# Optimization experiments

Hardware: AMD Instinct MI355X
Metric: run time of the kernel (lower is better)

## Reference

```python
import jax, jax.numpy as jnp
import numpy as np
import math

KEY_SIZE = 128  # init arg; scale = 1/sqrt(key_size)


def setup_inputs() -> dict:
    key = jax.random.key(0)
    kq, kk, kv = jax.random.split(key, 3)
    B, LQ, LK, D, DV = 16, 2048, 2048, 128, 128
    q = jax.random.normal(kq, (B, LQ, D), dtype=jnp.float32)
    k = jax.random.normal(kk, (B, LK, D), dtype=jnp.float32)
    v = jax.random.normal(kv, (B, LK, DV), dtype=jnp.float32)
    return {"q": q, "k": k, "v": v}


def reference(q, k, v):
    scale = 1.0 / math.sqrt(KEY_SIZE)
    # scores: [B, Lq, Lk]
    scores = jnp.einsum('bqd,bkd->bqk', q, k) * scale
    probs = jax.nn.softmax(scores, axis=-1)
    # dropout with p=0.0 is identity (eval-equivalent)
    return jnp.einsum('bqk,bkv->bqv', probs, v)
```

## Files before the change

kernel.cpp:

```cpp
#include <hip/hip_runtime.h>
#include <hip/hip_bf16.h>

typedef float f32x4 __attribute__((ext_vector_type(4)));
typedef float f32x16 __attribute__((ext_vector_type(16)));
typedef short bf16x8 __attribute__((ext_vector_type(8)));
typedef unsigned u32x4 __attribute__((ext_vector_type(4)));

constexpr int NB = 16, LQ = 2048, LK = 2048, D = 128, DV = 128;
constexpr int NTH = 32;
constexpr float SCALE = 0.08838834764831843f;
constexpr float LOG2E = 1.4426950408889634f;
constexpr float QSCALE = SCALE * LOG2E;
constexpr float SHIFT = 12.0f;

__device__ __forceinline__ unsigned short f2bfs(float f) {
  __hip_bfloat16 h = __float2bfloat16(f);
  return __builtin_bit_cast(unsigned short, h);
}

__device__ __forceinline__ unsigned short f2bf(float f) {
  unsigned int u = __float_as_uint(f);
  u += 0x7FFFu + ((u >> 16) & 1u);
  return (unsigned short)(u >> 16);
}

__device__ __forceinline__ int swz2(int row) {
  return (row ^ (row >> 1) ^ (row >> 3)) & 7;
}

__device__ __forceinline__ int swap23(int m) {
  return (m & ~12) | ((m & 4) << 1) | ((m & 8) >> 1);
}

typedef const __attribute__((address_space(1))) void* gas1_t;
typedef __attribute__((address_space(3))) void* las3_t;
__device__ __forceinline__ void gload16(const void* g, void* l) {
  __builtin_amdgcn_global_load_lds((gas1_t)g, (las3_t)l, 16, 0, 0);
}

__device__ __forceinline__ unsigned pk2(float lo, float hi) {
  unsigned short a = f2bfs(lo), b = f2bfs(hi);
  return (unsigned)a | ((unsigned)b << 16);
}

__device__ __forceinline__ void mk_pb(const f32x16& s, bf16x8& pe, bf16x8& po) {
  u32x4 e = {pk2(s[0], s[1]), pk2(s[2], s[3]), pk2(s[4], s[5]), pk2(s[6], s[7])};
  pe = __builtin_bit_cast(bf16x8, e);
  u32x4 od = {pk2(s[8], s[9]), pk2(s[10], s[11]), pk2(s[12], s[13]), pk2(s[14], s[15])};
  po = __builtin_bit_cast(bf16x8, od);
}

__global__ __launch_bounds__(256) void conv_k2(const float* __restrict__ kp,
                                               unsigned short* __restrict__ out) {
  __shared__ __align__(16) unsigned short tk[4096];
  const int T = blockIdx.x, b = blockIdx.y;
  const int tid = threadIdx.x;
  const int k = tid >> 3, cc = tid & 7, d0 = cc * 16;
  const float* src = kp + ((long)(b * LK) + 32 * T + k) * D + d0;
  f32x4 a0 = ((const f32x4*)src)[0];
  f32x4 a1 = ((const f32x4*)src)[1];
  f32x4 a2 = ((const f32x4*)src)[2];
  f32x4 a3 = ((const f32x4*)src)[3];
  bf16x8 r0, r1;
  #pragma unroll
  for (int j = 0; j < 4; ++j) {
    r0[j] = (short)f2bfs(a0[j]); r0[4 + j] = (short)f2bfs(a1[j]);
    r1[j] = (short)f2bfs(a2[j]); r1[4 + j] = (short)f2bfs(a3[j]);
  }
  const int rr = swap23(k);
  *(bf16x8*)&tk[(2 * cc) * 256 + rr * 8] = r0;
  *(bf16x8*)&tk[(2 * cc + 1) * 256 + rr * 8] = r1;
  __syncthreads();
  unsigned short* dst = out + ((long)(b * 64 + T)) * 4096 + tid * 16;
  *(bf16x8*)dst = *(const bf16x8*)&tk[tid * 16];
  *(bf16x8*)(dst + 8) = *(const bf16x8*)&tk[tid * 16 + 8];
}

__global__ __launch_bounds__(256) void conv_v2(const float* __restrict__ vp,
                                               unsigned short* __restrict__ out) {
  __shared__ __align__(16) unsigned short tv[4096];
  const int T = blockIdx.x, b = blockIdx.y;
  const int tid = threadIdx.x;
  const int k = tid >> 3, cc = tid & 7, d0 = cc * 16;
  const float* src = vp + ((long)(b * LK) + 32 * T + k) * DV + d0;
  f32x4 a0 = ((const f32x4*)src)[0];
  f32x4 a1 = ((const f32x4*)src)[1];
  f32x4 a2 = ((const f32x4*)src)[2];
  f32x4 a3 = ((const f32x4*)src)[3];
  unsigned short vals[16];
  #pragma unroll
  for (int j = 0; j < 4; ++j) {
    vals[j]      = f2bfs(a0[j]);
    vals[4 + j]  = f2bfs(a1[j]);
    vals[8 + j]  = f2bfs(a2[j]);
    vals[12 + j] = f2bfs(a3[j]);
  }
  const int vbase = (k >> 3) * 1024 + (k & 7);
  #pragma unroll
  for (int i = 0; i < 16; ++i)
    tv[vbase + (d0 + i) * 8] = vals[i];
  __syncthreads();
  unsigned short* dst = out + ((long)(b * 64 + T)) * 4096 + tid * 16;
  *(bf16x8*)dst = *(const bf16x8*)&tv[tid * 16];
  *(bf16x8*)(dst + 8) = *(const bf16x8*)&tv[tid * 16 + 8];
}

__global__ __launch_bounds__(256, 2) void attn_fwd9(
    const float* __restrict__ qp, const unsigned short* __restrict__ wsK2,
    const unsigned short* __restrict__ wsV2, float* __restrict__ op) {
  __shared__ __align__(16) unsigned short sm[32768];

  const int tid = threadIdx.x;
  const int wid = tid >> 6;
  const int h2  = wid >> 1;
  const int lane = tid & 63;
  const int q32 = lane & 31;
  const int hi  = lane >> 5;
  const int ht  = tid & 127;

  const int bid = blockIdx.x;
  const int sbid = (bid & 7) * 64 + (bid >> 3);
  const int b = sbid >> 5;
  const int qb = (sbid & 31) * 64;
  const int qwave = qb + (wid & 1) * 32;

  bf16x8 aq[8];
  {
    const float* qrow = qp + ((long)(b * LQ + qwave + q32)) * D + hi * 8;
    #pragma unroll
    for (int st = 0; st < 8; ++st) {
      f32x4 x0 = *(const f32x4*)(qrow + st * 16);
      f32x4 x1 = *(const f32x4*)(qrow + st * 16 + 4);
      #pragma unroll
      for (int j = 0; j < 4; ++j) {
        aq[st][j]     = (short)f2bfs(x0[j] * QSCALE);
        aq[st][4 + j] = (short)f2bfs(x1[j] * QSCALE);
      }
    }
  }
  __builtin_amdgcn_sched_barrier(0);

  const int lbase = h2 * 16384;
  const unsigned short* kps = wsK2 + ((long)(b * 64 + h2 * 32)) * 4096;
  const unsigned short* vps = wsV2 + ((long)(b * 64 + h2 * 32)) * 4096;

  auto stage = [&](int buf, int t) {
    const long toff = (long)t * 4096;
    const int lb = lbase + buf * 8192;
    #pragma unroll
    for (int it = 0; it < 4; ++it) {
      const int ci = it * 128 + ht;
      gload16(kps + toff + ci * 8, &sm[lb + ci * 8]);
    }
    #pragma unroll
    for (int it = 0; it < 4; ++it) {
      const int ci = it * 128 + ht;
      gload16(vps + toff + ci * 8, &sm[lb + 4096 + ci * 8]);
    }
  };

  stage(0, 0);
  stage(1, 1);

  f32x16 o[4];
  #pragma unroll
  for (int mt = 0; mt < 4; ++mt) o[mt] = (f32x16){};
  float l_s = 0.f;

  const int kub = lbase + hi * 256 + q32 * 8;
  const int vub = lbase + 4096 + hi * 1024 + q32 * 8;

  asm volatile("s_waitcnt vmcnt(8)" ::: "memory");
  __builtin_amdgcn_sched_barrier(0);
  __builtin_amdgcn_s_barrier();
  __builtin_amdgcn_sched_barrier(0);

  f32x16 s_cur;
  #pragma unroll
  for (int i = 0; i < 16; ++i) s_cur[i] = -SHIFT;
  #pragma unroll
  for (int st = 0; st < 8; ++st) {
    bf16x8 k0 = *(const bf16x8*)&sm[kub + st * 512];
    s_cur = __builtin_amdgcn_mfma_f32_32x32x16_bf16(k0, aq[st], s_cur, 0, 0, 0);
  }
  bf16x8 vf[8];
  #pragma unroll
  for (int ks = 0; ks < 2; ++ks)
    #pragma unroll
    for (int mt = 0; mt < 4; ++mt)
      vf[ks * 4 + mt] = *(const bf16x8*)&sm[vub + ks * 2048 + mt * 256];

  asm volatile("s_waitcnt lgkmcnt(0)" ::: "memory");
  __builtin_amdgcn_sched_barrier(0);
  __builtin_amdgcn_s_barrier();
  __builtin_amdgcn_sched_barrier(0);
  stage(0, 2);

  for (int t = 1; t < NTH; ++t) {
    if (t < NTH - 1) {
      asm volatile("s_waitcnt vmcnt(8)" ::: "memory");
    } else {
      asm volatile("s_waitcnt vmcnt(0)" ::: "memory");
    }
    __builtin_amdgcn_sched_barrier(0);
    __builtin_amdgcn_s_barrier();
    __builtin_amdgcn_sched_barrier(0);

    const int cur = t & 1;
    const int kb = kub + cur * 8192;
    const int vb = vub + cur * 8192;

    f32x16 s_new;
    #pragma unroll
    for (int i = 0; i < 16; ++i) s_new[i] = -SHIFT;
    __builtin_amdgcn_s_setprio(1);
    #pragma unroll
    for (int st = 0; st < 8; ++st) {
      bf16x8 k0 = *(const bf16x8*)&sm[kb + st * 512];
      s_new = __builtin_amdgcn_mfma_f32_32x32x16_bf16(k0, aq[st], s_new, 0, 0, 0);
    }
    __builtin_amdgcn_s_setprio(0);

    #pragma unroll
    for (int i = 0; i < 16; ++i) s_cur[i] = exp2f(s_cur[i]);
    float s8[8];
    #pragma unroll
    for (int i = 0; i < 8; ++i) s8[i] = s_cur[i] + s_cur[i + 8];
    float sum = ((s8[0] + s8[1]) + (s8[2] + s8[3])) +
                ((s8[4] + s8[5]) + (s8[6] + s8[7]));
    l_s += sum + __shfl_xor(sum, 32);
    bf16x8 pb0, pb1;
    mk_pb(s_cur, pb0, pb1);

    __builtin_amdgcn_s_setprio(1);
    #pragma unroll
    for (int mt = 0; mt < 4; ++mt)
      o[mt] = __builtin_amdgcn_mfma_f32_32x32x16_bf16(vf[mt], pb0, o[mt], 0, 0, 0);
    #pragma unroll
    for (int mt = 0; mt < 4; ++mt)
      o[mt] = __builtin_amdgcn_mfma_f32_32x32x16_bf16(vf[4 + mt], pb1, o[mt], 0, 0, 0);
    __builtin_amdgcn_s_setprio(0);

    #pragma unroll
    for (int ks = 0; ks < 2; ++ks)
      #pragma unroll
      for (int mt = 0; mt < 4; ++mt)
        vf[ks * 4 + mt] = *(const bf16x8*)&sm[vb + ks * 2048 + mt * 256];

    asm volatile("s_waitcnt lgkmcnt(0)" ::: "memory");
    __builtin_amdgcn_sched_barrier(0);
    __builtin_amdgcn_s_barrier();
    __builtin_amdgcn_sched_barrier(0);
    if (t + 2 < NTH) stage(cur, t + 2);

    s_cur = s_new;
  }

  {
    #pragma unroll
    for (int i = 0; i < 16; ++i) s_cur[i] = exp2f(s_cur[i]);
    float s8[8];
    #pragma unroll
    for (int i = 0; i < 8; ++i) s8[i] = s_cur[i] + s_cur[i + 8];
    float sum = ((s8[0] + s8[1]) + (s8[2] + s8[3])) +
                ((s8[4] + s8[5]) + (s8[6] + s8[7]));
    l_s += sum + __shfl_xor(sum, 32);
    bf16x8 pb0, pb1;
    mk_pb(s_cur, pb0, pb1);
    #pragma unroll
    for (int mt = 0; mt < 4; ++mt)
      o[mt] = __builtin_amdgcn_mfma_f32_32x32x16_bf16(vf[mt], pb0, o[mt], 0, 0, 0);
    #pragma unroll
    for (int mt = 0; mt < 4; ++mt)
      o[mt] = __builtin_amdgcn_mfma_f32_32x32x16_bf16(vf[4 + mt], pb1, o[mt], 0, 0, 0);
  }

  float* scr = (float*)sm;
  float* wreg = scr + (size_t)(wid & 1) * 4352;
  __syncthreads();
  if (h2 == 1) {
    #pragma unroll
    for (int j4 = 0; j4 < 16; ++j4) {
      const int mt = j4 >> 2, a = j4 & 3;
      f32x4 v = {o[mt][4 * a], o[mt][4 * a + 1], o[mt][4 * a + 2], o[mt][4 * a + 3]};
      *(f32x4*)&wreg[lane * 64 + ((j4 ^ (lane & 15)) << 2)] = v;
    }
    wreg[4096 + lane] = l_s;
  }
  __syncthreads();
  if (h2 == 0) {
    const float l1 = wreg[4096 + lane];
    const float inv = 1.f / (l_s + l1);
    float* dst = op + ((long)(b * LQ + qwave + q32)) * DV;
    #pragma unroll
    for (int j4 = 0; j4 < 16; ++j4) {
      const int mt = j4 >> 2, a = j4 & 3;
      f32x4 pv = *(const f32x4*)&wreg[lane * 64 + ((j4 ^ (lane & 15)) << 2)];
      f32x4 r;
      #pragma unroll
      for (int i = 0; i < 4; ++i) r[i] = (o[mt][4 * a + i] + pv[i]) * inv;
      *(f32x4*)&dst[32 * mt + 8 * a + 4 * hi] = r;
    }
  }
}

__device__ __forceinline__ int swzc(int row, int c16) {
  return c16 ^ ((row ^ (row >> 3)) & 7);
}

__global__ __launch_bounds__(256, 2) void attn_fwd(
    const float* __restrict__ qp, const float* __restrict__ kp,
    const float* __restrict__ vp, float* __restrict__ op) {
  __shared__ __align__(16) unsigned short smm[28672];
  const int tid = threadIdx.x, wid = tid >> 6, lane = tid & 63;
  const int g = lane >> 4, c = lane & 15;
  const int b = blockIdx.y, qb = blockIdx.x * 64;
  const float* qg = qp + ((long)b * LQ + qb) * D;
  const float* kg = kp + (long)b * LK * D;
  const float* vg = vp + (long)b * LK * DV;
  #pragma unroll
  for (int it = 0; it < 4; ++it) {
    int ch = it * 256 + tid, row = ch >> 4, c16 = ch & 15;
    const float* src = qg + row * D + c16 * 8;
    f32x4 f0 = *(const f32x4*)(src);
    f32x4 f1 = *(const f32x4*)(src + 4);
    bf16x8 fr;
    #pragma unroll
    for (int j = 0; j < 4; ++j) {
      fr[j] = (short)f2bf(f0[j] * SCALE);
      fr[4 + j] = (short)f2bf(f1[j] * SCALE);
    }
    *(bf16x8*)&smm[row * 128 + swzc(row, c16) * 8] = fr;
  }
  __syncthreads();
  bf16x8 aq[4];
  #pragma unroll
  for (int ks = 0; ks < 4; ++ks) {
    int row = wid * 16 + c;
    aq[ks] = *(const bf16x8*)&smm[row * 128 + swzc(row, ks * 4 + g) * 8];
  }
  f32x4 o[8]; f32x4 fz = {0.f, 0.f, 0.f, 0.f};
  #pragma unroll
  for (int i = 0; i < 8; ++i) o[i] = fz;
  float m_r[4] = {-1e30f, -1e30f, -1e30f, -1e30f};
  float l_r[4] = {0.f, 0.f, 0.f, 0.f};
  const int pbase = 24576 + wid * 1024;
  for (int kv0 = 0; kv0 < LK; kv0 += 64) {
    __syncthreads();
    const float* ksrc = kg + (long)kv0 * D;
    #pragma unroll
    for (int it = 0; it < 4; ++it) {
      int ch = it * 256 + tid, row = ch >> 4, c16 = ch & 15;
      const float* src = ksrc + row * D + c16 * 8;
      f32x4 f0 = *(const f32x4*)(src);
      f32x4 f1 = *(const f32x4*)(src + 4);
      bf16x8 fr;
      #pragma unroll
      for (int j = 0; j < 4; ++j) { fr[j] = (short)f2bf(f0[j]); fr[4 + j] = (short)f2bf(f1[j]); }
      *(bf16x8*)&smm[8192 + row * 128 + swzc(row, c16) * 8] = fr;
    }
    {
      const float* vsrc = vg + (long)kv0 * DV;
      int dvq = (tid & 31) * 4, kg8 = tid >> 5;
      f32x4 col[8];
      #pragma unroll
      for (int j = 0; j < 8; ++j) col[j] = *(const f32x4*)(vsrc + (kg8 * 8 + j) * DV + dvq);
      #pragma unroll
      for (int i = 0; i < 4; ++i) {
        int dv = dvq + i;
        bf16x8 fr;
        #pragma unroll
        for (int j = 0; j < 8; ++j) fr[j] = (short)f2bf(col[j][i]);
        *(bf16x8*)&smm[16384 + dv * 64 + swzc(dv, kg8) * 8] = fr;
      }
    }
    __syncthreads();
    f32x4 s[4];
    #pragma unroll
    for (int i = 0; i < 4; ++i) s[i] = fz;
    #pragma unroll
    for (int ks = 0; ks < 4; ++ks) {
      #pragma unroll
      for (int t = 0; t < 4; ++t) {
        int row = t * 16 + c;
        bf16x8 bk = *(const bf16x8*)&smm[8192 + row * 128 + swzc(row, ks * 4 + g) * 8];
        s[t] = __builtin_amdgcn_mfma_f32_16x16x32_bf16(aq[ks], bk, s[t], 0, 0, 0);
      }
    }
    #pragma unroll
    for (int r = 0; r < 4; ++r) {
      float pm = fmaxf(fmaxf(s[0][r], s[1][r]), fmaxf(s[2][r], s[3][r]));
      pm = fmaxf(pm, __shfl_xor(pm, 1));
      pm = fmaxf(pm, __shfl_xor(pm, 2));
      pm = fmaxf(pm, __shfl_xor(pm, 4));
      pm = fmaxf(pm, __shfl_xor(pm, 8));
      float mn = fmaxf(m_r[r], pm);
      float al = exp2f((m_r[r] - mn) * LOG2E);
      float sum = 0.f;
      #pragma unroll
      for (int t = 0; t < 4; ++t) {
        float p = exp2f((s[t][r] - mn) * LOG2E);
        s[t][r] = p; sum += p;
      }
      sum += __shfl_xor(sum, 1); sum += __shfl_xor(sum, 2);
      sum += __shfl_xor(sum, 4); sum += __shfl_xor(sum, 8);
      l_r[r] = l_r[r] * al + sum; m_r[r] = mn;
      #pragma unroll
      for (int dvt = 0; dvt < 8; ++dvt) o[dvt][r] *= al;
    }
    #pragma unroll
    for (int t = 0; t < 4; ++t)
      #pragma unroll
      for (int r = 0; r < 4; ++r) {
        int row = g * 4 + r, colx = c + 16 * t;
        smm[pbase + row * 64 + swzc(row, colx >> 3) * 8 + (colx & 7)] = f2bf(s[t][r]);
      }
    #pragma unroll
    for (int ks = 0; ks < 2; ++ks) {
      bf16x8 pa = *(const bf16x8*)&smm[pbase + c * 64 + swzc(c, ks * 4 + g) * 8];
      #pragma unroll
      for (int dvt = 0; dvt < 8; ++dvt) {
        int row = dvt * 16 + c;
        bf16x8 vb2 = *(const bf16x8*)&smm[16384 + row * 64 + swzc(row, ks * 4 + g) * 8];
        o[dvt] = __builtin_amdgcn_mfma_f32_16x16x32_bf16(pa, vb2, o[dvt], 0, 0, 0);
      }
    }
  }
  float* dst = op + ((long)b * LQ + qb + wid * 16) * DV;
  #pragma unroll
  for (int r = 0; r < 4; ++r) {
    float inv = 1.f / l_r[r];
    #pragma unroll
    for (int dvt = 0; dvt < 8; ++dvt)
      dst[(g * 4 + r) * DV + dvt * 16 + c] = o[dvt][r] * inv;
  }
}

extern "C" void kernel_launch(void* const* d_in, const int* in_sizes, int n_in,
                              void* d_out, int out_size, void* d_ws, size_t ws_size,
                              hipStream_t stream) {
  const float* q = (const float*)d_in[0];
  const float* k = (const float*)d_in[1];
  const float* v = (const float*)d_in[2];
  float* out = (float*)d_out;

  const size_t kelems = (size_t)NB * LK * D;
  const size_t need = kelems * 2 * 2;
  if (ws_size >= need) {
    unsigned short* wsK2 = (unsigned short*)d_ws;
    unsigned short* wsV2 = wsK2 + kelems;
    conv_k2<<<dim3(LK / 32, NB), dim3(256), 0, stream>>>(k, wsK2);
    conv_v2<<<dim3(LK / 32, NB), dim3(256), 0, stream>>>(v, wsV2);
    attn_fwd9<<<dim3(NB * LQ / 64), dim3(256), 0, stream>>>(q, wsK2, wsV2, out);
  } else {
    attn_fwd<<<dim3(LQ / 64, NB), dim3(256), 0, stream>>>(q, k, v, out);
  }
}
```

Before: 75.93 us.

## Load V fragments directly from global into registers, stage only K in LDS

The V tiles are no longer staged through shared memory. Each lane reads its V MFMA fragments straight from the pre-swizzled global workspace into registers, one tile ahead, using ping-pong register sets (vfA/vfB) and a manually unrolled two-step loop. This cuts LDS usage roughly in half and removes the LDS write/read traffic for V. In exchange it adds register pressure and exposes global-load latency on the V path, where vmcnt waits now cover both the K async copies and the direct V loads.

```diff
diff --git a/kernel.cpp b/kernel.cpp
--- a/kernel.cpp
+++ b/kernel.cpp
@@ -105,10 +105,10 @@
   *(bf16x8*)(dst + 8) = *(const bf16x8*)&tv[tid * 16 + 8];
 }
 
-__global__ __launch_bounds__(256, 2) void attn_fwd9(
+__global__ __launch_bounds__(256, 2) void attn_fwd10(
     const float* __restrict__ qp, const unsigned short* __restrict__ wsK2,
     const unsigned short* __restrict__ wsV2, float* __restrict__ op) {
-  __shared__ __align__(16) unsigned short sm[32768];
+  __shared__ __align__(16) unsigned short sm[17408];
 
   const int tid = threadIdx.x;
   const int wid = tid >> 6;
@@ -140,27 +140,23 @@
   }
   __builtin_amdgcn_sched_barrier(0);
 
-  const int lbase = h2 * 16384;
+  const int lbase = h2 * 8192;
   const unsigned short* kps = wsK2 + ((long)(b * 64 + h2 * 32)) * 4096;
   const unsigned short* vps = wsV2 + ((long)(b * 64 + h2 * 32)) * 4096;
-
-  auto stage = [&](int buf, int t) {
+  const unsigned short* vgb = vps + hi * 1024 + q32 * 8;
+
+  auto stageK = [&](int buf, int t) {
     const long toff = (long)t * 4096;
-    const int lb = lbase + buf * 8192;
+    const int lb = lbase + buf * 4096;
     #pragma unroll
     for (int it = 0; it < 4; ++it) {
       const int ci = it * 128 + ht;
       gload16(kps + toff + ci * 8, &sm[lb + ci * 8]);
     }
-    #pragma unroll
-    for (int it = 0; it < 4; ++it) {
-      const int ci = it * 128 + ht;
-      gload16(vps + toff + ci * 8, &sm[lb + 4096 + ci * 8]);
-    }
   };
 
-  stage(0, 0);
-  stage(1, 1);
+  stageK(0, 0);
+  stageK(1, 1);
 
   f32x16 o[4];
   #pragma unroll
@@ -168,37 +164,36 @@
   float l_s = 0.f;
 
   const int kub = lbase + hi * 256 + q32 * 8;
-  const int vub = lbase + 4096 + hi * 1024 + q32 * 8;
-
-  asm volatile("s_waitcnt vmcnt(8)" ::: "memory");
+
+  f32x16 sA, sB;
+  bf16x8 vfA[8], vfB[8];
+
+  asm volatile("s_waitcnt vmcnt(4)" ::: "memory");
   __builtin_amdgcn_sched_barrier(0);
   __builtin_amdgcn_s_barrier();
   __builtin_amdgcn_sched_barrier(0);
-
-  f32x16 s_cur;
-  #pragma unroll
-  for (int i = 0; i < 16; ++i) s_cur[i] = -SHIFT;
+  #pragma unroll
+  for (int i = 0; i < 16; ++i) sA[i] = -SHIFT;
   #pragma unroll
   for (int st = 0; st < 8; ++st) {
     bf16x8 k0 = *(const bf16x8*)&sm[kub + st * 512];
-    s_cur = __builtin_amdgcn_mfma_f32_32x32x16_bf16(k0, aq[st], s_cur, 0, 0, 0);
-  }
-  bf16x8 vf[8];
+    sA = __builtin_amdgcn_mfma_f32_32x32x16_bf16(k0, aq[st], sA, 0, 0, 0);
+  }
   #pragma unroll
   for (int ks = 0; ks < 2; ++ks)
     #pragma unroll
     for (int mt = 0; mt < 4; ++mt)
-      vf[ks * 4 + mt] = *(const bf16x8*)&sm[vub + ks * 2048 + mt * 256];
-
+      vfA[ks * 4 + mt] = *(const bf16x8*)(vgb + ks * 2048 + mt * 256);
   asm volatile("s_waitcnt lgkmcnt(0)" ::: "memory");
   __builtin_amdgcn_sched_barrier(0);
   __builtin_amdgcn_s_barrier();
   __builtin_amdgcn_sched_barrier(0);
-  stage(0, 2);
-
-  for (int t = 1; t < NTH; ++t) {
+  stageK(0, 2);
+
+  auto body = [&](int t, f32x16& s_prev, f32x16& s_next,
+                  bf16x8 (&v_prev)[8], bf16x8 (&v_next)[8]) {
     if (t < NTH - 1) {
-      asm volatile("s_waitcnt vmcnt(8)" ::: "memory");
+      asm volatile("s_waitcnt vmcnt(4)" ::: "memory");
     } else {
       asm volatile("s_waitcnt vmcnt(0)" ::: "memory");
     }
@@ -206,73 +201,77 @@
     __builtin_amdgcn_s_barrier();
     __builtin_amdgcn_sched_barrier(0);
 
-    const int cur = t & 1;
-    const int kb = kub + cur * 8192;
-    const int vb = vub + cur * 8192;
-
-    f32x16 s_new;
-    #pragma unroll
-    for (int i = 0; i < 16; ++i) s_new[i] = -SHIFT;
+    const int kb = kub + (t & 1) * 4096;
+
+    #pragma unroll
+    for (int i = 0; i < 16; ++i) s_next[i] = -SHIFT;
     __builtin_amdgcn_s_setprio(1);
     #pragma unroll
     for (int st = 0; st < 8; ++st) {
       bf16x8 k0 = *(const bf16x8*)&sm[kb + st * 512];
-      s_new = __builtin_amdgcn_mfma_f32_32x32x16_bf16(k0, aq[st], s_new, 0, 0, 0);
+      s_next = __builtin_amdgcn_mfma_f32_32x32x16_bf16(k0, aq[st], s_next, 0, 0, 0);
     }
     __builtin_amdgcn_s_setprio(0);
 
-    #pragma unroll
-    for (int i = 0; i < 16; ++i) s_cur[i] = exp2f(s_cur[i]);
+    const unsigned short* vt = vgb + (long)t * 4096;
+    #pragma unroll
+    for (int ks = 0; ks < 2; ++ks)
+      #pragma unroll
+      for (int mt = 0; mt < 4; ++mt)
+        v_next[ks * 4 + mt] = *(const bf16x8*)(vt + ks * 2048 + mt * 256);
+
+    #pragma unroll
+    for (int i = 0; i < 16; ++i) s_prev[i] = exp2f(s_prev[i]);
     float s8[8];
     #pragma unroll
-    for (int i = 0; i < 8; ++i) s8[i] = s_cur[i] + s_cur[i + 8];
+    for (int i = 0; i < 8; ++i) s8[i] = s_prev[i] + s_prev[i + 8];
     float sum = ((s8[0] + s8[1]) + (s8[2] + s8[3])) +
                 ((s8[4] + s8[5]) + (s8[6] + s8[7]));
     l_s += sum + __shfl_xor(sum, 32);
     bf16x8 pb0, pb1;
-    mk_pb(s_cur, pb0, pb1);
+    mk_pb(s_prev, pb0, pb1);
 
     __builtin_amdgcn_s_setprio(1);
     #pragma unroll
     for (int mt = 0; mt < 4; ++mt)
-      o[mt] = __builtin_amdgcn_mfma_f32_32x32x16_bf16(vf[mt], pb0, o[mt], 0, 0, 0);
+      o[mt] = __builtin_amdgcn_mfma_f32_32x32x16_bf16(v_prev[mt], pb0, o[mt], 0, 0, 0);
     #pragma unroll
     for (int mt = 0; mt < 4; ++mt)
-      o[mt] = __builtin_amdgcn_mfma_f32_32x32x16_bf16(vf[4 + mt], pb1, o[mt], 0, 0, 0);
+      o[mt] = __builtin_amdgcn_mfma_f32_32x32x16_bf16(v_prev[4 + mt], pb1, o[mt], 0, 0, 0);
     __builtin_amdgcn_s_setprio(0);
-
-    #pragma unroll
-    for (int ks = 0; ks < 2; ++ks)
-      #pragma unroll
-      for (int mt = 0; mt < 4; ++mt)
-        vf[ks * 4 + mt] = *(const bf16x8*)&sm[vb + ks * 2048 + mt * 256];
 
     asm volatile("s_waitcnt lgkmcnt(0)" ::: "memory");
     __builtin_amdgcn_sched_barrier(0);
     __builtin_amdgcn_s_barrier();
     __builtin_amdgcn_sched_barrier(0);
-    if (t + 2 < NTH) stage(cur, t + 2);
-
-    s_cur = s_new;
-  }
+    if (t + 2 < NTH) stageK(t & 1, t + 2);
+  };
+
+  for (int tt = 1; tt < NTH - 1; tt += 2) {
+    body(tt,     sA, sB, vfA, vfB);
+    body(tt + 1, sB, sA, vfB, vfA);
+  }
+  body(NTH - 1, sA, sB, vfA, vfB);
 
   {
-    #pragma unroll
-    for (int i = 0; i < 16; ++i) s_cur[i] = exp2f(s_cur[i]);
+    asm volatile("s_waitcnt vmcnt(0)" ::: "memory");
+    __builtin_amdgcn_sched_barrier(0);
+    #pragma unroll
+    for (int i = 0; i < 16; ++i) sB[i] = exp2f(sB[i]);
     float s8[8];
     #pragma unroll
-    for (int i = 0; i < 8; ++i) s8[i] = s_cur[i] + s_cur[i + 8];
+    for (int i = 0; i < 8; ++i) s8[i] = sB[i] + sB[i + 8];
     float sum = ((s8[0] + s8[1]) + (s8[2] + s8[3])) +
                 ((s8[4] + s8[5]) + (s8[6] + s8[7]));
     l_s += sum + __shfl_xor(sum, 32);
     bf16x8 pb0, pb1;
-    mk_pb(s_cur, pb0, pb1);
+    mk_pb(sB, pb0, pb1);
     #pragma unroll
     for (int mt = 0; mt < 4; ++mt)
-      o[mt] = __builtin_amdgcn_mfma_f32_32x32x16_bf16(vf[mt], pb0, o[mt], 0, 0, 0);
+      o[mt] = __builtin_amdgcn_mfma_f32_32x32x16_bf16(vfB[mt], pb0, o[mt], 0, 0, 0);
     #pragma unroll
     for (int mt = 0; mt < 4; ++mt)
-      o[mt] = __builtin_amdgcn_mfma_f32_32x32x16_bf16(vf[4 + mt], pb1, o[mt], 0, 0, 0);
+      o[mt] = __builtin_amdgcn_mfma_f32_32x32x16_bf16(vfB[4 + mt], pb1, o[mt], 0, 0, 0);
   }
 
   float* scr = (float*)sm;
@@ -451,7 +450,7 @@
     unsigned short* wsV2 = wsK2 + kelems;
     conv_k2<<<dim3(LK / 32, NB), dim3(256), 0, stream>>>(k, wsK2);
     conv_v2<<<dim3(LK / 32, NB), dim3(256), 0, stream>>>(v, wsV2);
-    attn_fwd9<<<dim3(NB * LQ / 64), dim3(256), 0, stream>>>(q, wsK2, wsV2, out);
+    attn_fwd10<<<dim3(NB * LQ / 64), dim3(256), 0, stream>>>(q, wsK2, wsV2, out);
   } else {
     attn_fwd<<<dim3(LQ / 64, NB), dim3(256), 0, stream>>>(q, k, v, out);
   }
```

New measurement: 73.65 us. 1.03x faster.
